# Optimization experiments

Hardware: AMD Instinct MI355X
Metric: run time of the kernel (lower is better)

## Reference

```python
import jax, jax.numpy as jnp
import numpy as np

TEMPERATURE = 0.7

def setup_inputs() -> dict:
    key = jax.random.key(0)
    k1, k2 = jax.random.split(key)
    B, S, D = 32, 1024, 768
    features = jax.random.normal(k1, (B, S, D), dtype=jnp.float32)
    labels = jax.random.randint(k2, (B, S), 0, 16).astype(jnp.int64)
    return {"features": features, "labels": labels}


def reference(features, labels):
    # Faithful vectorization of the nested-loop SupConLoss.
    # For anchor i in group P (label k), with N_i = S - |P| negatives (N_i > 0):
    #   logNegL_i = log( sum_{n not in P} exp( (f_i.f_n / T / sqrt(D)) / N_i ) )
    #   contrib_i = -(1/|P|) * sum_{j in P, j>i} ( f_i.f_j / T / sqrt(D) - logNegL_i )
    # loss = sum over batches/groups/anchors contrib / S, returned as (1,1).
    B, S, D = features.shape
    dim_norm = jnp.sqrt(jnp.asarray(D, dtype=features.dtype))
    # [B,S,S] scaled similarity: (f_i . f_j) / temperature / sqrt(D)
    sim = jnp.einsum('bid,bjd->bij', features, features) / (TEMPERATURE * dim_norm)

    same = labels[:, :, None] == labels[:, None, :]            # [B,S,S] same-label mask
    group_size = jnp.sum(same, axis=-1)                        # [B,S] |P| (includes self)
    num_neg = S - group_size                                   # [B,S] N_i
    has_neg = num_neg > 0
    safe_nn = jnp.maximum(num_neg, 1).astype(features.dtype)   # avoid div by 0

    # negative logits: exp(sim / N_i) summed over negatives of anchor i
    neg_exp = jnp.where(~same, jnp.exp(sim / safe_nn[:, :, None]), 0.0)
    neg_logits = jnp.sum(neg_exp, axis=-1)                     # [B,S]
    log_neg = jnp.log(jnp.where(has_neg, neg_logits, 1.0))     # [B,S]

    # positives strictly after anchor (j > i) with same label
    tri = jnp.triu(jnp.ones((S, S), dtype=bool), k=1)          # j > i
    later = same & tri[None, :, :]                             # [B,S,S]
    pos_sum = jnp.sum(jnp.where(later, sim, 0.0), axis=-1)     # [B,S] sum_j sim[i,j]
    n_later = jnp.sum(later, axis=-1).astype(features.dtype)   # [B,S] count of j>i pairs

    per_anchor = -(pos_sum - n_later * log_neg) / group_size.astype(features.dtype)
    per_anchor = jnp.where(has_neg, per_anchor, 0.0)

    loss = jnp.sum(per_anchor) / S
    return loss.reshape(1, 1)
```

## Files before the change

### kernel.cpp

```cpp
#include <hip/hip_runtime.h>
#include <hip/hip_bf16.h>

#define NB 32
#define NS 1024
#define ND 768
#define BS_TOT (NB * NS)

#define SCALE 0.05154913f


__global__ __launch_bounds__(256) void meta_kernel(
    const int* __restrict__ lr, int i64, int* __restrict__ orderP,
    int* __restrict__ startG, int* __restrict__ cntI,
    float* __restrict__ out) {
  __shared__ int labs[NS];
  __shared__ int hist[256][17];
  __shared__ int cnt[16];
  __shared__ int startL[16];
  int b = blockIdx.x, t = threadIdx.x;
  for (int i = t; i < NS; i += 256) {
    int gi = b * NS + i;
    labs[i] = (i64 ? lr[2 * gi] : lr[gi]) & 15;
  }
#pragma unroll
  for (int L = 0; L < 16; ++L) hist[t][L] = 0;
  __syncthreads();
  int lab4[4];
#pragma unroll
  for (int e = 0; e < 4; ++e) {
    lab4[e] = labs[t * 4 + e];
    hist[t][lab4[e]]++;
  }
  __syncthreads();
#pragma unroll
  for (int off = 1; off < 256; off <<= 1) {
    int tmp[16];
#pragma unroll
    for (int L = 0; L < 16; ++L) tmp[L] = (t >= off) ? hist[t - off][L] : 0;
    __syncthreads();
#pragma unroll
    for (int L = 0; L < 16; ++L) hist[t][L] += tmp[L];
    __syncthreads();
  }
  if (t < 16) cnt[t] = hist[255][t];
  __syncthreads();
  if (t == 0) {
    int s = 0;
#pragma unroll
    for (int L = 0; L < 16; ++L) {
      startL[L] = s;
      s += cnt[L];
    }
  }
  __syncthreads();
#pragma unroll
  for (int e = 0; e < 4; ++e) {
    int i = t * 4 + e;
    int lab = lab4[e];
    int later_own = 0;
#pragma unroll
    for (int e2 = 0; e2 < 4; ++e2)
      if (e2 > e && lab4[e2] == lab) later_own++;
    int rank = hist[t][lab] - 1 - later_own;
    int nlat = cnt[lab] - 1 - rank;
    orderP[b * NS + startL[lab] + rank] = i | (nlat << 12);
  }
  if (t < 16) {
    startG[b * 16 + t] = startL[t];
    cntI[b * 16 + t] = cnt[t];
  }
  if (b == 0 && t == 0) out[0] = 0.0f;
}

__global__ __launch_bounds__(192) void gsum_kernel(
    const float* __restrict__ feat, const int* __restrict__ orderP,
    const int* __restrict__ startG, const int* __restrict__ cntI,
    float* __restrict__ g, float* __restrict__ h, float* __restrict__ ssq) {
  const int b = blockIdx.x >> 5, lab = (blockIdx.x >> 1) & 15;
  const int half = blockIdx.x & 1;
  const int gstart = startG[b * 16 + lab];
  const int gn = cntI[b * 16 + lab];
  const int h0 = (gn + 1) >> 1;
  const int start = gstart + (half ? h0 : 0);
  const int n = half ? (gn - h0) : h0;
  const int t = threadIdx.x;
  __shared__ int ord[512];
  for (int i = t; i < n; i += 192) ord[i] = orderP[b * NS + start + i];
  __syncthreads();
  const float* fb = feat + (size_t)b * NS * ND;
  float gx = 0.f, gy = 0.f, gz = 0.f, gw = 0.f;
  float hx = 0.f, hy = 0.f, hz = 0.f, hw = 0.f;
  float sq = 0.f;
  const int full = n & ~15;
  for (int r = 0; r < full; r += 16) {
    float4 v[16];
    float wt[16];
#pragma unroll
    for (int u = 0; u < 16; ++u) {
      const int p = __builtin_amdgcn_readfirstlane(ord[r + u]);
      wt[u] = (float)(p >> 12);
      v[u] = *(const float4*)(fb + (size_t)(p & 1023) * ND + 4 * t);
    }
#pragma unroll
    for (int u = 0; u < 16; ++u) {
      gx += v[u].x; gy += v[u].y; gz += v[u].z; gw += v[u].w;
      hx += wt[u] * v[u].x; hy += wt[u] * v[u].y;
      hz += wt[u] * v[u].z; hw += wt[u] * v[u].w;
      sq += v[u].x * v[u].x + v[u].y * v[u].y + v[u].z * v[u].z +
            v[u].w * v[u].w;
    }
  }
  if (full < n) {
    const int rem = n - full;
    float4 v[16];
    float wt[16], msk[16];
#pragma unroll
    for (int u = 0; u < 16; ++u) {
      int rr = full + (u < rem ? u : rem - 1);
      const int p = __builtin_amdgcn_readfirstlane(ord[rr]);
      wt[u] = (float)(p >> 12);
      msk[u] = (u < rem) ? 1.0f : 0.0f;
      v[u] = *(const float4*)(fb + (size_t)(p & 1023) * ND + 4 * t);
    }
#pragma unroll
    for (int u = 0; u < 16; ++u) {
      const float m = msk[u];
      gx += m * v[u].x; gy += m * v[u].y; gz += m * v[u].z; gw += m * v[u].w;
      const float mw = m * wt[u];
      hx += mw * v[u].x; hy += mw * v[u].y;
      hz += mw * v[u].z; hw += mw * v[u].w;
      sq += m * (v[u].x * v[u].x + v[u].y * v[u].y + v[u].z * v[u].z +
                 v[u].w * v[u].w);
    }
  }
  const size_t base = ((size_t)((b * 16 + lab) * 2 + half)) * ND + 4 * t;
  *(float4*)(g + base) = make_float4(gx, gy, gz, gw);
  *(float4*)(h + base) = make_float4(hx, hy, hz, hw);
#pragma unroll
  for (int m = 1; m < 64; m <<= 1) sq += __shfl_xor(sq, m);
  __shared__ float red[3];
  if ((t & 63) == 0) red[t >> 6] = sq;
  __syncthreads();
  if (t == 0) ssq[(b * 16 + lab) * 2 + half] = red[0] + red[1] + red[2];
}

__global__ __launch_bounds__(192) void final_kernel(
    const float* __restrict__ g, const float* __restrict__ h,
    const float* __restrict__ ssq, const int* __restrict__ cntI,
    float* __restrict__ out) {
  const int b = blockIdx.x, t = threadIdx.x;
  const int w = t >> 6, l = t & 63;
  const float* gb = g + (size_t)b * 16 * 2 * ND;
  const float* hb = h + (size_t)b * 16 * 2 * ND;
  float4 gv[16], hv[16];
#pragma unroll
  for (int P = 0; P < 16; ++P) {
    float4 a0 = *(const float4*)(gb + (P * 2 + 0) * ND + 4 * t);
    float4 a1 = *(const float4*)(gb + (P * 2 + 1) * ND + 4 * t);
    gv[P] = make_float4(a0.x + a1.x, a0.y + a1.y, a0.z + a1.z, a0.w + a1.w);
    float4 c0 = *(const float4*)(hb + (P * 2 + 0) * ND + 4 * t);
    float4 c1 = *(const float4*)(hb + (P * 2 + 1) * ND + 4 * t);
    hv[P] = make_float4(c0.x + c1.x, c0.y + c1.y, c0.z + c1.z, c0.w + c1.w);
  }
  float4 G4 = make_float4(0.f, 0.f, 0.f, 0.f);
#pragma unroll
  for (int P = 0; P < 16; ++P) {
    G4.x += gv[P].x; G4.y += gv[P].y; G4.z += gv[P].z; G4.w += gv[P].w;
  }
  float hd[16], gg[16];
#pragma unroll
  for (int P = 0; P < 16; ++P) {
    hd[P] = hv[P].x * (G4.x - gv[P].x) + hv[P].y * (G4.y - gv[P].y) +
            hv[P].z * (G4.z - gv[P].z) + hv[P].w * (G4.w - gv[P].w);
    gg[P] = gv[P].x * gv[P].x + gv[P].y * gv[P].y + gv[P].z * gv[P].z +
            gv[P].w * gv[P].w;
  }
#pragma unroll
  for (int m = 1; m < 64; m <<= 1)
#pragma unroll
    for (int P = 0; P < 16; ++P) {
      hd[P] += __shfl_xor(hd[P], m);
      gg[P] += __shfl_xor(gg[P], m);
    }
  __shared__ float rh[3][16], rg[3][16];
  if (l == 0)
#pragma unroll
    for (int P = 0; P < 16; ++P) {
      rh[w][P] = hd[P];
      rg[w][P] = gg[P];
    }
  __syncthreads();
  if (t < 16) {
    float shd = rh[0][t] + rh[1][t] + rh[2][t];
    float sgg = rg[0][t] + rg[1][t] + rg[2][t];
    float c = (float)cntI[b * 16 + t];
    float nn = (float)NS - c;
    float val = 0.0f;
    if (c > 0.5f && nn > 0.5f) {
      float invGS = 1.0f / c;
      float sumNlat = 0.5f * c * (c - 1.0f);
      float sq = ssq[(b * 16 + t) * 2] + ssq[(b * 16 + t) * 2 + 1];
      val = invGS * (sumNlat * logf(nn) + (SCALE / (nn * nn)) * shd +
                     0.5f * SCALE * (sq - sgg));
    }
#pragma unroll
    for (int m = 1; m < 16; m <<= 1) val += __shfl_xor(val, m);
    if (t == 0) atomicAdd(out, val * (1.0f / NS));
  }
}

extern "C" void kernel_launch(void* const* d_in, const int* in_sizes, int n_in,
                              void* d_out, int out_size, void* d_ws,
                              size_t ws_size, hipStream_t stream) {
  (void)out_size;
  (void)ws_size;
  const float* feat = (const float*)d_in[0];
  const int* labels = (const int*)d_in[1];
  float* out = (float*)d_out;
  const int i64 = (n_in > 1 && in_sizes[1] == BS_TOT * 4) ? 0 : 1;

  char* w = (char*)d_ws;
  int* orderP = (int*)w;
  size_t off = (size_t)BS_TOT * 4;
  int* startG = (int*)(w + off);
  off += (size_t)NB * 16 * 4;
  int* cntI = (int*)(w + off);
  off += (size_t)NB * 16 * 4;
  float* g = (float*)(w + off);
  off += (size_t)NB * 16 * 2 * ND * 4;
  float* h = (float*)(w + off);
  off += (size_t)NB * 16 * 2 * ND * 4;
  float* ssq = (float*)(w + off);
  off += (size_t)NB * 16 * 2 * 4;

  meta_kernel<<<NB, 256, 0, stream>>>(labels, i64, orderP, startG, cntI, out);
  gsum_kernel<<<NB * 32, 192, 0, stream>>>(feat, orderP, startG, cntI, g, h,
                                           ssq);
  final_kernel<<<NB, 192, 0, stream>>>(g, h, ssq, cntI, out);
}
```

Measured before the change: 163.4 us.

## Split gsum rows across waves with per-wave full-row accumulation and LDS reduction

Each of the three waves in gsum_kernel now owns every third row of the group and accumulates the full 768-wide row (three float4 per lane), where before all 192 threads walked the same rows and each covered a column slice. Partial g/h sums from waves 1 and 2 go through shared memory and wave 0 adds them before writing out. This gives each wave its own independent rows to load, aiming for more memory-level parallelism and less serialization on the shared row index. The cost is about 12KB of shared memory, more registers (24 accumulators plus 24 float4 loads in flight), and an extra reduction step.

```diff
diff --git a/kernel.cpp b/kernel.cpp
--- a/kernel.cpp
+++ b/kernel.cpp
@@ -83,65 +83,82 @@
   const int h0 = (gn + 1) >> 1;
   const int start = gstart + (half ? h0 : 0);
   const int n = half ? (gn - h0) : h0;
-  const int t = threadIdx.x;
+  const int t = threadIdx.x, w = t >> 6, l = t & 63;
   __shared__ int ord[512];
+  __shared__ float red[2][2][ND];
+  __shared__ float rss[3];
   for (int i = t; i < n; i += 192) ord[i] = orderP[b * NS + start + i];
   __syncthreads();
   const float* fb = feat + (size_t)b * NS * ND;
-  float gx = 0.f, gy = 0.f, gz = 0.f, gw = 0.f;
-  float hx = 0.f, hy = 0.f, hz = 0.f, hw = 0.f;
-  float sq = 0.f;
-  const int full = n & ~15;
-  for (int r = 0; r < full; r += 16) {
-    float4 v[16];
-    float wt[16];
-#pragma unroll
-    for (int u = 0; u < 16; ++u) {
-      const int p = __builtin_amdgcn_readfirstlane(ord[r + u]);
+  const int nw = (n > w) ? ((n - 1 - w) / 3 + 1) : 0;
+  float ga[12], ha[12];
+#pragma unroll
+  for (int d = 0; d < 12; ++d) ga[d] = ha[d] = 0.0f;
+  float sq = 0.0f;
+  for (int k0 = 0; k0 < nw; k0 += 8) {
+    float4 v[8][3];
+    float wt[8], mk[8];
+#pragma unroll
+    for (int u = 0; u < 8; ++u) {
+      const int k = k0 + u;
+      const int kc = (k < nw) ? k : (nw - 1);
+      const int p = ord[w + 3 * kc];
       wt[u] = (float)(p >> 12);
-      v[u] = *(const float4*)(fb + (size_t)(p & 1023) * ND + 4 * t);
-    }
-#pragma unroll
-    for (int u = 0; u < 16; ++u) {
-      gx += v[u].x; gy += v[u].y; gz += v[u].z; gw += v[u].w;
-      hx += wt[u] * v[u].x; hy += wt[u] * v[u].y;
-      hz += wt[u] * v[u].z; hw += wt[u] * v[u].w;
-      sq += v[u].x * v[u].x + v[u].y * v[u].y + v[u].z * v[u].z +
-            v[u].w * v[u].w;
-    }
-  }
-  if (full < n) {
-    const int rem = n - full;
-    float4 v[16];
-    float wt[16], msk[16];
-#pragma unroll
-    for (int u = 0; u < 16; ++u) {
-      int rr = full + (u < rem ? u : rem - 1);
-      const int p = __builtin_amdgcn_readfirstlane(ord[rr]);
-      wt[u] = (float)(p >> 12);
-      msk[u] = (u < rem) ? 1.0f : 0.0f;
-      v[u] = *(const float4*)(fb + (size_t)(p & 1023) * ND + 4 * t);
-    }
-#pragma unroll
-    for (int u = 0; u < 16; ++u) {
-      const float m = msk[u];
-      gx += m * v[u].x; gy += m * v[u].y; gz += m * v[u].z; gw += m * v[u].w;
-      const float mw = m * wt[u];
-      hx += mw * v[u].x; hy += mw * v[u].y;
-      hz += mw * v[u].z; hw += mw * v[u].w;
-      sq += m * (v[u].x * v[u].x + v[u].y * v[u].y + v[u].z * v[u].z +
-                 v[u].w * v[u].w);
-    }
-  }
-  const size_t base = ((size_t)((b * 16 + lab) * 2 + half)) * ND + 4 * t;
-  *(float4*)(g + base) = make_float4(gx, gy, gz, gw);
-  *(float4*)(h + base) = make_float4(hx, hy, hz, hw);
+      mk[u] = (k < nw) ? 1.0f : 0.0f;
+      const float* rp = fb + (size_t)(p & 1023) * ND + 4 * l;
+#pragma unroll
+      for (int c = 0; c < 3; ++c) v[u][c] = *(const float4*)(rp + 256 * c);
+    }
+#pragma unroll
+    for (int u = 0; u < 8; ++u) {
+      const float m = mk[u];
+      const float mw = mk[u] * wt[u];
+#pragma unroll
+      for (int c = 0; c < 3; ++c) {
+        ga[c * 4 + 0] += m * v[u][c].x;
+        ga[c * 4 + 1] += m * v[u][c].y;
+        ga[c * 4 + 2] += m * v[u][c].z;
+        ga[c * 4 + 3] += m * v[u][c].w;
+        ha[c * 4 + 0] += mw * v[u][c].x;
+        ha[c * 4 + 1] += mw * v[u][c].y;
+        ha[c * 4 + 2] += mw * v[u][c].z;
+        ha[c * 4 + 3] += mw * v[u][c].w;
+        sq += m * (v[u][c].x * v[u][c].x + v[u][c].y * v[u][c].y +
+                   v[u][c].z * v[u][c].z + v[u][c].w * v[u][c].w);
+      }
+    }
+  }
+  if (w > 0) {
+#pragma unroll
+    for (int c = 0; c < 3; ++c) {
+      *(float4*)&red[w - 1][0][4 * l + 256 * c] =
+          make_float4(ga[c * 4], ga[c * 4 + 1], ga[c * 4 + 2], ga[c * 4 + 3]);
+      *(float4*)&red[w - 1][1][4 * l + 256 * c] =
+          make_float4(ha[c * 4], ha[c * 4 + 1], ha[c * 4 + 2], ha[c * 4 + 3]);
+    }
+  }
 #pragma unroll
   for (int m = 1; m < 64; m <<= 1) sq += __shfl_xor(sq, m);
-  __shared__ float red[3];
-  if ((t & 63) == 0) red[t >> 6] = sq;
-  __syncthreads();
-  if (t == 0) ssq[(b * 16 + lab) * 2 + half] = red[0] + red[1] + red[2];
+  if (l == 0) rss[w] = sq;
+  __syncthreads();
+  if (w == 0) {
+    const size_t base = ((size_t)((b * 16 + lab) * 2 + half)) * ND + 4 * l;
+#pragma unroll
+    for (int c = 0; c < 3; ++c) {
+      float4 r0 = *(const float4*)&red[0][0][4 * l + 256 * c];
+      float4 r1 = *(const float4*)&red[1][0][4 * l + 256 * c];
+      *(float4*)(g + base + 256 * c) =
+          make_float4(ga[c * 4] + r0.x + r1.x, ga[c * 4 + 1] + r0.y + r1.y,
+                      ga[c * 4 + 2] + r0.z + r1.z, ga[c * 4 + 3] + r0.w + r1.w);
+      float4 s0 = *(const float4*)&red[0][1][4 * l + 256 * c];
+      float4 s1 = *(const float4*)&red[1][1][4 * l + 256 * c];
+      *(float4*)(h + base + 256 * c) =
+          make_float4(ha[c * 4] + s0.x + s1.x, ha[c * 4 + 1] + s0.y + s1.y,
+                      ha[c * 4 + 2] + s0.z + s1.z, ha[c * 4 + 3] + s0.w + s1.w);
+    }
+    if (t == 0)
+      ssq[(b * 16 + lab) * 2 + half] = rss[0] + rss[1] + rss[2];
+  }
 }
 
 __global__ __launch_bounds__(192) void final_kernel(
```

New measurement: 164.4 us. No clear change (+0.6%).
